# Kernel tuning notes

Hardware: AMD Instinct MI355X
Metric: run time of the kernel (lower is better)

The kernel has to match this reference:

```python
import jax, jax.numpy as jnp
import numpy as np

N_NODES = 7823
N_DRUG = 708
N_TARGET = 1512
N_DISEASE = N_NODES - N_DRUG - N_TARGET  # 5603
FEAT = 1024
HID = 512
OUT = 256
LN_EPS = 1e-5


def _adapter_params(key, in_dim, out_dim):
    k1, k2 = jax.random.split(key)
    s1 = (2.0 / (in_dim + out_dim)) ** 0.5
    return dict(
        W=jax.random.normal(k1, (out_dim, in_dim), jnp.float32) * s1,
        b=jnp.zeros((out_dim,), jnp.float32),
        g=jnp.ones((out_dim,), jnp.float32),
        beta=jnp.zeros((out_dim,), jnp.float32),
        Wr=jax.random.normal(k2, (out_dim, in_dim), jnp.float32) * s1,
        br=jnp.zeros((out_dim,), jnp.float32),
    )


def setup_inputs() -> dict:
    key = jax.random.key(0)
    ks = jax.random.split(key, 12)
    inp = {
        'drug_feats': jax.random.normal(ks[0], (N_DRUG, FEAT), jnp.float32),
        'target_feats': jax.random.normal(ks[1], (N_TARGET, FEAT), jnp.float32),
        'disease_feats': jax.random.normal(ks[2], (N_DISEASE, FEAT), jnp.float32),
        'drug_adjs': jax.random.uniform(ks[3], (2, N_NODES, N_NODES), jnp.float32),
        'target_adjs': jax.random.uniform(ks[4], (2, N_NODES, N_NODES), jnp.float32),
    }
    # adapters
    for name, k in [('dA', ks[5]), ('tA', ks[6]), ('sA', ks[7])]:
        p = _adapter_params(k, FEAT, HID)
        for pn, pv in p.items():
            inp[name + '_' + pn] = pv
    # GCN weights: gc1 [HID,OUT], gc2 [OUT,OUT], uniform(-1/sqrt(out),1/sqrt(out))
    stdv = 1.0 / (OUT ** 0.5)
    inp['dG_W1'] = jax.random.uniform(ks[8], (HID, OUT), jnp.float32, -stdv, stdv)
    inp['dG_W2'] = jax.random.uniform(ks[9], (OUT, OUT), jnp.float32, -stdv, stdv)
    inp['tG_W1'] = jax.random.uniform(ks[10], (HID, OUT), jnp.float32, -stdv, stdv)
    inp['tG_W2'] = jax.random.uniform(ks[11], (OUT, OUT), jnp.float32, -stdv, stdv)
    inp['dG_a'] = jnp.full((1,), 0.25, jnp.float32)  # PReLU init
    inp['tG_a'] = jnp.full((1,), 0.25, jnp.float32)
    return inp


def _layernorm(x, g, b):
    m = x.mean(-1, keepdims=True)
    v = x.var(-1, keepdims=True)
    return (x - m) / jnp.sqrt(v + LN_EPS) * g + b


def _adapter(x, W, b, g, beta, Wr, br):
    out = jax.nn.relu(_layernorm(x @ W.T + b, g, beta))
    return out + x @ Wr.T + br


def _prelu(x, a):
    return jnp.where(x >= 0, x, a * x)


def _gcn(x, adj, W1, W2, a):
    h = _prelu(adj @ (x @ W1), a)
    Z = adj @ (h @ W2)
    # nn.LayerNorm(Z.size()) normalizes over the WHOLE tensor, no affine
    return (Z - Z.mean()) / jnp.sqrt(Z.var() + LN_EPS)


def reference(drug_feats, target_feats, disease_feats, drug_adjs, target_adjs,
              dA_W, dA_b, dA_g, dA_beta, dA_Wr, dA_br,
              tA_W, tA_b, tA_g, tA_beta, tA_Wr, tA_br,
              sA_W, sA_b, sA_g, sA_beta, sA_Wr, sA_br,
              dG_W1, dG_W2, dG_a, tG_W1, tG_W2, tG_a):
    h_drug = jax.nn.elu(_adapter(drug_feats, dA_W, dA_b, dA_g, dA_beta, dA_Wr, dA_br))
    h_target = jax.nn.elu(_adapter(target_feats, tA_W, tA_b, tA_g, tA_beta, tA_Wr, tA_br))
    h_disease = jax.nn.elu(_adapter(disease_feats, sA_W, sA_b, sA_g, sA_beta, sA_Wr, sA_br))
    x_all = jnp.concatenate([h_drug, h_target, h_disease], axis=0)  # [7823, HID]
    adj_d = drug_adjs.mean(0)
    adj_t = target_adjs.mean(0)
    z_drug = _gcn(x_all, adj_d, dG_W1, dG_W2, dG_a)[:N_DRUG]
    z_target = _gcn(x_all, adj_t, tG_W1, tG_W2, tG_a)[N_DRUG:N_DRUG + N_TARGET]
    z_drug = z_drug / (jnp.linalg.norm(z_drug, axis=1, keepdims=True) + 1e-8)
    z_target = z_target / (jnp.linalg.norm(z_target, axis=1, keepdims=True) + 1e-8)
    return (z_drug, z_target)
```

## Files before the change

kernel.cpp:

```cpp
#include <hip/hip_runtime.h>
#include <hip/hip_bf16.h>
#include <stdint.h>

typedef __attribute__((ext_vector_type(8))) short short8;
typedef __attribute__((ext_vector_type(4))) float f32x4;

#define N_DRUG 708
#define N_TGT  1512
#define N_NODES 7823
#define N_D_T  2220
#define KPAD   8192
#define MROWP  7936
#define NTOT   2002688
#define NSPLIT 4
#define PLANE  61199329LL
#define ADJSTR ((long long)MROWP*KPAD)
#define BTSTR  ((long long)256*KPAD)
#define PSTR   ((long long)NSPLIT*NTOT)

__device__ __forceinline__ unsigned short f2bf(float f) {
  union { float f; unsigned int i; } v; v.f = f;
  unsigned int r = v.i + 0x7FFF + ((v.i >> 16) & 1);
  return (unsigned short)(r >> 16);
}

__device__ __forceinline__ int4 pack8(const float v[8]) {
  union { int4 i4; unsigned short u[8]; } r;
  #pragma unroll
  for (int j = 0; j < 8; j++) r.u[j] = f2bf(v[j]);
  return r.i4;
}


__global__ __launch_bounds__(256) void cast_wc(
    const float* __restrict__ w0, const float* __restrict__ wr0,
    const float* __restrict__ w1, const float* __restrict__ wr1,
    const float* __restrict__ w2, const float* __restrict__ wr2,
    unsigned short* __restrict__ Wc)
{
  long long i4 = ((long long)blockIdx.x*256 + threadIdx.x)*4;
  int g  = (int)(i4 >> 20);
  int rr = (int)((i4 >> 10) & 1023);
  int c  = (int)(i4 & 1023);
  const float* src = (g==0) ? (rr<512?w0:wr0) : (g==1) ? (rr<512?w1:wr1) : (rr<512?w2:wr2);
  float4 f = *(const float4*)(src + (long long)(rr & 511)*1024 + c);
  ushort4 v; v.x=f2bf(f.x); v.y=f2bf(f.y); v.z=f2bf(f.z); v.w=f2bf(f.w);
  *(ushort4*)&Wc[i4] = v;
}

__global__ __launch_bounds__(256) void transpose_cast(
    const float* __restrict__ src, unsigned short* __restrict__ dst, int R, int C)
{
  int i = blockIdx.x*256 + threadIdx.x;
  if (i >= R*C) return;
  int r = i / C, c = i - r*C;
  dst[c*R + r] = f2bf(src[i]);
}

__global__ __launch_bounds__(256) void mean_cast_row(
    const float* __restrict__ A0, const float* __restrict__ A1,
    unsigned short* __restrict__ D)
{
  int row = blockIdx.x;
  const float* p0 = (blockIdx.y ? A1 : A0) + (long long)row*N_NODES;
  const float* p1 = p0 + PLANE;
  unsigned short* d = D + (long long)blockIdx.y*ADJSTR + (long long)row*KPAD;

  for (int c = threadIdx.x*8; c < 7816; c += 2048) {
    float4 a0 = *(const float4*)(p0+c);
    float4 a1 = *(const float4*)(p0+c+4);
    float4 b0 = *(const float4*)(p1+c);
    float4 b1 = *(const float4*)(p1+c+4);
    float v[8] = {0.5f*(a0.x+b0.x), 0.5f*(a0.y+b0.y), 0.5f*(a0.z+b0.z), 0.5f*(a0.w+b0.w),
                  0.5f*(a1.x+b1.x), 0.5f*(a1.y+b1.y), 0.5f*(a1.z+b1.z), 0.5f*(a1.w+b1.w)};
    *(int4*)(d + c) = pack8(v);
  }
  int t = threadIdx.x;
  if (t < 7) {
    int c = 7816 + t;
    d[c] = f2bf(0.5f*(p0[c] + p1[c]));
  }
}

__global__ __launch_bounds__(512, 2) void spmmK(
    const unsigned short* __restrict__ Abase,
    const unsigned short* __restrict__ Bbase,
    float* __restrict__ parts)
{
  __shared__ __align__(16) unsigned short Bs[2][128*256];

  int bid = (blockIdx.x & 7)*62 + (blockIdx.x >> 3);
  int grp = bid / 62;
  int q   = bid % 62;
  int b  = grp >> 2;
  int ks = grp & 3;
  int mt = q >> 1, nt = q & 1;

  const unsigned short* A  = Abase + b*ADJSTR;
  const unsigned short* BT = Bbase + b*BTSTR;
  int m0 = mt*256, n0 = nt*128;
  int kt0 = ks*32;

  int tid = threadIdx.x, lane = tid & 63, w = tid >> 6;
  int grow = m0 + w*32 + (lane&15);
  long long rA0 = (long long)grow*KPAD + (lane>>4)*8;

  f32x4 acc[2][8] = {};

  int srow[8], sslot[8];
  #pragma unroll
  for (int i=0;i<8;i++){ int c = i*512 + tid; srow[i] = c>>5; sslot[i] = c&31; }

  int4 breg[8];
  auto loadB = [&](int sub){
    long long kb = (long long)kt0*64 + sub*256;
    #pragma unroll
    for (int i=0;i<8;i++)
      breg[i] = *(const int4*)(BT + (long long)(n0+srow[i])*KPAD + kb + sslot[i]*8);
  };
  auto storeB = [&](unsigned short* buf){
    #pragma unroll
    for (int i=0;i<8;i++)
      *(int4*)(buf + srow[i]*256 + (sslot[i]^(srow[i]&7))*8) = breg[i];
  };
  auto loadA = [&](int g, int4* a){
    const unsigned short* p = A + rA0 + (long long)g*64;
    a[0] = *(const int4*)(p);
    a[1] = *(const int4*)(p + 16*KPAD);
    a[2] = *(const int4*)(p + 32);
    a[3] = *(const int4*)(p + 16*KPAD + 32);
  };
  auto compute = [&](int lt, const int4* a, const unsigned short* buf){
    #pragma unroll
    for (int kk=0; kk<2; ++kk) {
      short8 bv[8];
      #pragma unroll
      for (int nf=0; nf<8; ++nf) {
        int row = nf*16 + (lane&15);
        int sl  = (lt*8 + kk*4 + (lane>>4)) ^ (lane&7);
        bv[nf] = *(const short8*)&buf[row*256 + sl*8];
      }
      #pragma unroll
      for (int mf=0; mf<2; ++mf) {
        short8 av = *(const short8*)&a[kk*2+mf];
        #pragma unroll
        for (int nf=0; nf<8; ++nf)
          acc[mf][nf] = __builtin_amdgcn_mfma_f32_16x16x32_bf16(av, bv[nf], acc[mf][nf], 0, 0, 0);
      }
    }
  };

  int gmax = kt0 + 31;
  int4 a0[4], a1[4], a2[4], a3[4];

  loadB(0);
  loadA(kt0+0, a0);
  loadA(kt0+1, a1);
  loadA(kt0+2, a2);
  loadA(kt0+3, a3);
  storeB(&Bs[0][0]);
  loadB(1);
  asm volatile("s_waitcnt lgkmcnt(0)" ::: "memory");
  __builtin_amdgcn_s_barrier();
  __builtin_amdgcn_sched_barrier(0);

  int cur = 0;
  for (int sub = 0; sub < 8; ++sub) {
    const unsigned short* Bc = &Bs[cur][0];
    int g = kt0 + sub*4;
    compute(0, a0, Bc); loadA(min(g+4, gmax), a0);
    compute(1, a1, Bc); loadA(min(g+5, gmax), a1);
    compute(2, a2, Bc); loadA(min(g+6, gmax), a2);
    compute(3, a3, Bc); loadA(min(g+7, gmax), a3);
    if (sub < 7) {
      __builtin_amdgcn_s_barrier();
      __builtin_amdgcn_sched_barrier(0);
      storeB(&Bs[cur^1][0]);
      loadB(min(sub+2, 7));
      asm volatile("s_waitcnt lgkmcnt(0)" ::: "memory");
      __builtin_amdgcn_s_barrier();
      __builtin_amdgcn_sched_barrier(0);
      cur ^= 1;
    }
  }

  float* P = parts + b*PSTR + (long long)ks*NTOT;
  #pragma unroll
  for (int mf=0; mf<2; ++mf) {
    int mb = m0 + w*32 + mf*16 + ((lane>>4)<<2);
    #pragma unroll
    for (int i=0;i<4;i++){
      int m = mb + i;
      if (m < N_NODES) {
        #pragma unroll
        for (int nf=0; nf<8; ++nf) {
          int n = n0 + nf*16 + (lane&15);
          P[(long long)m*256 + n] = acc[mf][nf][i];
        }
      }
    }
  }
}

#define BN 256
#define BK 64

__global__ __launch_bounds__(512, 4) void gemmS(
    const unsigned short* __restrict__ Abase, long long a_bstr, int lda,
    const unsigned short* __restrict__ Bbase, long long b_bstr, int ldb,
    int m_cnt, int tiles_m, int ktiles,
    unsigned short* __restrict__ CTb, long long ct_bstr, int ldct)
{
  __shared__ __align__(16) unsigned short As[64*BK];
  __shared__ __align__(16) unsigned short Bs[BN*BK];

  int bid = blockIdx.x;
  int b   = bid / tiles_m;
  int tm  = bid % tiles_m;

  const unsigned short* A  = Abase + b*a_bstr;
  const unsigned short* BT = Bbase + b*b_bstr;

  int m0 = tm*64;
  int tid = threadIdx.x;
  int lane = tid & 63, w = tid >> 6;
  int wm = (w >> 2)*32, wn = (w & 3)*64;

  f32x4 acc[2][4] = {};

  int arow, aslot, brow[4], bslot[4];
  { int c = tid; arow = c>>3; aslot = c&7; }
  #pragma unroll
  for (int i=0;i<4;i++){ int c = i*512 + tid; brow[i] = c>>3; bslot[i] = c&7; }

  int4 ra, rb[4];
  auto loadAB = [&](int kt){
    int gr = m0 + arow; if (gr > m_cnt-1) gr = m_cnt-1;
    ra = *(const int4*)(A + (long long)gr*lda + kt*BK + aslot*8);
    #pragma unroll
    for (int i=0;i<4;i++)
      rb[i] = *(const int4*)(BT + (long long)brow[i]*ldb + kt*BK + bslot[i]*8);
  };
  auto storeAB = [&](){
    *(int4*)(As + arow*BK + (aslot^(arow&7))*8) = ra;
    #pragma unroll
    for (int i=0;i<4;i++)
      *(int4*)(Bs + brow[i]*BK + (bslot[i]^(brow[i]&7))*8) = rb[i];
  };

  loadAB(0);
  for (int kt = 0; kt < ktiles; ++kt) {
    __syncthreads();
    storeAB();
    __syncthreads();
    if (kt+1 < ktiles) loadAB(kt+1);
    #pragma unroll
    for (int kk=0; kk<2; ++kk) {
      short8 av[2], bv[4];
      #pragma unroll
      for (int x=0;x<2;x++){
        int row = wm + x*16 + (lane&15);
        int slot = kk*4 + (lane>>4);
        av[x] = *(const short8*)&As[row*BK + (slot^(row&7))*8];
      }
      #pragma unroll
      for (int x=0;x<4;x++){
        int row = wn + x*16 + (lane&15);
        int slot = kk*4 + (lane>>4);
        bv[x] = *(const short8*)&Bs[row*BK + (slot^(row&7))*8];
      }
      #pragma unroll
      for (int mf=0; mf<2; ++mf)
        #pragma unroll
        for (int nf=0; nf<4; ++nf)
          acc[mf][nf] = __builtin_amdgcn_mfma_f32_16x16x32_bf16(av[mf], bv[nf], acc[mf][nf], 0, 0, 0);
    }
  }

  unsigned short* CT = CTb + b*ct_bstr;
  #pragma unroll
  for (int nf=0; nf<4; ++nf) {
    int n = wn + nf*16 + (lane&15);
    #pragma unroll
    for (int mf=0; mf<2; ++mf) {
      int mb = m0 + wm + mf*16 + ((lane>>4)<<2);
      ushort4 v;
      v.x = (mb+0 < m_cnt) ? f2bf(acc[mf][nf][0]) : (unsigned short)0;
      v.y = (mb+1 < m_cnt) ? f2bf(acc[mf][nf][1]) : (unsigned short)0;
      v.z = (mb+2 < m_cnt) ? f2bf(acc[mf][nf][2]) : (unsigned short)0;
      v.w = (mb+3 < m_cnt) ? f2bf(acc[mf][nf][3]) : (unsigned short)0;
      *(ushort4*)&CT[(long long)n*ldct + mb] = v;
    }
  }
}

__global__ __launch_bounds__(512, 4) void adapt_gemm(
    const float* __restrict__ f0, const float* __restrict__ f1, const float* __restrict__ f2,
    const unsigned short* __restrict__ Wc, float* __restrict__ C1)
{
  __shared__ __align__(16) unsigned short As[64*BK];
  __shared__ __align__(16) unsigned short Bs[BN*BK];

  int bid = blockIdx.x;
  int tn = bid & 3, tq = bid >> 2;
  int g, lt, m_cnt, gstart;
  if (tq < 12)      { g=0; lt=tq;    m_cnt=N_DRUG;           gstart=0; }
  else if (tq < 36) { g=1; lt=tq-12; m_cnt=N_TGT;            gstart=N_DRUG; }
  else              { g=2; lt=tq-36; m_cnt=N_NODES-N_D_T;    gstart=N_D_T; }
  const float* A = (g==0) ? f0 : (g==1) ? f1 : f2;
  const unsigned short* BT = Wc + (long long)g*1024*1024;

  int m0 = lt*64, n0 = tn*BN;
  int tid = threadIdx.x;
  int lane = tid & 63, w = tid >> 6;
  int wm = (w >> 2)*32, wn = (w & 3)*64;

  f32x4 acc[2][4] = {};

  int arow, aslot, brow[4], bslot[4];
  { int c = tid; arow = c>>3; aslot = c&7; }
  #pragma unroll
  for (int i=0;i<4;i++){ int c = i*512 + tid; brow[i] = c>>3; bslot[i] = c&7; }

  int4 ra, rb[4];
  auto loadAB = [&](int kt){
    int gr = m0 + arow; if (gr > m_cnt-1) gr = m_cnt-1;
    const float* p = A + (long long)gr*1024 + kt*BK + aslot*8;
    float4 q0 = *(const float4*)p;
    float4 q1 = *(const float4*)(p+4);
    float v[8] = {q0.x,q0.y,q0.z,q0.w,q1.x,q1.y,q1.z,q1.w};
    ra = pack8(v);
    #pragma unroll
    for (int i=0;i<4;i++)
      rb[i] = *(const int4*)(BT + (long long)(n0 + brow[i])*1024 + kt*BK + bslot[i]*8);
  };
  auto storeAB = [&](){
    *(int4*)(As + arow*BK + (aslot^(arow&7))*8) = ra;
    #pragma unroll
    for (int i=0;i<4;i++)
      *(int4*)(Bs + brow[i]*BK + (bslot[i]^(brow[i]&7))*8) = rb[i];
  };

  loadAB(0);
  for (int kt = 0; kt < 16; ++kt) {
    __syncthreads();
    storeAB();
    __syncthreads();
    if (kt+1 < 16) loadAB(kt+1);
    #pragma unroll
    for (int kk=0; kk<2; ++kk) {
      short8 av[2], bv[4];
      #pragma unroll
      for (int x=0;x<2;x++){
        int row = wm + x*16 + (lane&15);
        int slot = kk*4 + (lane>>4);
        av[x] = *(const short8*)&As[row*BK + (slot^(row&7))*8];
      }
      #pragma unroll
      for (int x=0;x<4;x++){
        int row = wn + x*16 + (lane&15);
        int slot = kk*4 + (lane>>4);
        bv[x] = *(const short8*)&Bs[row*BK + (slot^(row&7))*8];
      }
      #pragma unroll
      for (int mf=0; mf<2; ++mf)
        #pragma unroll
        for (int nf=0; nf<4; ++nf)
          acc[mf][nf] = __builtin_amdgcn_mfma_f32_16x16x32_bf16(av[mf], bv[nf], acc[mf][nf], 0, 0, 0);
    }
  }

  #pragma unroll
  for (int mf=0; mf<2; ++mf) {
    int mb = m0 + wm + mf*16 + ((lane>>4)<<2);
    #pragma unroll
    for (int i=0;i<4;i++){
      int m = mb + i;
      if (m < m_cnt) {
        #pragma unroll
        for (int nf=0; nf<4; ++nf) {
          int n = n0 + wn + nf*16 + (lane&15);
          C1[(long long)(gstart+m)*1024 + n] = acc[mf][nf][i];
        }
      }
    }
  }
}


__global__ __launch_bounds__(256) void adapter_fuse(
    const float* __restrict__ C1,
    const float* __restrict__ b0, const float* __restrict__ g0, const float* __restrict__ be0, const float* __restrict__ br0,
    const float* __restrict__ b1, const float* __restrict__ g1, const float* __restrict__ be1, const float* __restrict__ br1,
    const float* __restrict__ b2, const float* __restrict__ g2, const float* __restrict__ be2, const float* __restrict__ br2,
    unsigned short* __restrict__ xall)
{
  int r = blockIdx.x;
  const float *b, *g, *be, *br;
  if (r < N_DRUG)     { b=b0; g=g0; be=be0; br=br0; }
  else if (r < N_D_T) { b=b1; g=g1; be=be1; br=br1; }
  else                { b=b2; g=g2; be=be2; br=br2; }
  int t = threadIdx.x;
  const float* row = C1 + (long long)r*1024;
  float ya = row[t]       + b[t];
  float yb = row[t + 256] + b[t + 256];
  float s = ya + yb, q = ya*ya + yb*yb;
  #pragma unroll
  for (int o=32;o;o>>=1){ s += __shfl_down(s,o); q += __shfl_down(q,o); }
  __shared__ float ss[4], qq[4];
  if ((t & 63) == 0) { ss[t>>6]=s; qq[t>>6]=q; }
  __syncthreads();
  float S = ss[0]+ss[1]+ss[2]+ss[3];
  float Q = qq[0]+qq[1]+qq[2]+qq[3];
  float mean = S * (1.f/512.f);
  float var  = Q * (1.f/512.f) - mean*mean;
  float inv  = rsqrtf(var + 1e-5f);
  float za = fmaxf((ya-mean)*inv*g[t]     + be[t],     0.f);
  float zb = fmaxf((yb-mean)*inv*g[t+256] + be[t+256], 0.f);
  float ha = za + row[512 + t] + br[t];
  float hb = zb + row[768 + t] + br[t + 256];
  ha = (ha > 0.f) ? ha : (expf(ha) - 1.f);
  hb = (hb > 0.f) ? hb : (expf(hb) - 1.f);
  xall[(long long)r*512 + t]       = f2bf(ha);
  xall[(long long)r*512 + t + 256] = f2bf(hb);
}

__global__ __launch_bounds__(256) void reduce_prelu2(
    const float* __restrict__ parts, const float* __restrict__ a0, const float* __restrict__ a1,
    unsigned short* __restrict__ h)
{
  int b = blockIdx.y;
  long long i = (long long)blockIdx.x*256 + threadIdx.x;
  const float* P = parts + b*PSTR;
  float s = 0.f;
  #pragma unroll
  for (int p=0;p<NSPLIT;p++) s += P[(long long)p*NTOT + i];
  float a = (b ? a1 : a0)[0];
  h[b*(long long)NTOT + i] = f2bf(s >= 0.f ? s : a*s);
}

__global__ __launch_bounds__(256) void reduce_stats2(
    const float* __restrict__ parts, float* __restrict__ Z, float* __restrict__ sp)
{
  int b = blockIdx.y;
  long long i = (long long)blockIdx.x*256 + threadIdx.x;
  const float* P = parts + b*PSTR;
  float s = 0.f;
  #pragma unroll
  for (int p=0;p<NSPLIT;p++) s += P[(long long)p*NTOT + i];
  Z[b*(long long)NTOT + i] = s;
  float a = s, q = s*s;
  #pragma unroll
  for (int o=32;o;o>>=1){ a += __shfl_down(a,o); q += __shfl_down(q,o); }
  __shared__ float ss[4], qq[4];
  int t = threadIdx.x;
  if ((t&63)==0){ ss[t>>6]=a; qq[t>>6]=q; }
  __syncthreads();
  if (t==0) {
    sp[(long long)b*2*N_NODES + 2*blockIdx.x]   = ss[0]+ss[1]+ss[2]+ss[3];
    sp[(long long)b*2*N_NODES + 2*blockIdx.x+1] = qq[0]+qq[1]+qq[2]+qq[3];
  }
}

__global__ __launch_bounds__(256) void stats_final2(
    const float* __restrict__ sp, float* __restrict__ stats)
{
  int b = blockIdx.x;
  const float* S = sp + (long long)b*2*N_NODES;
  int t = threadIdx.x;
  float s = 0.f, q = 0.f;
  for (int i=t; i<N_NODES; i+=256){ s += S[2*i]; q += S[2*i+1]; }
  #pragma unroll
  for (int o=32;o;o>>=1){ s += __shfl_down(s,o); q += __shfl_down(q,o); }
  __shared__ float ss[4], qq[4];
  if ((t&63)==0){ ss[t>>6]=s; qq[t>>6]=q; }
  __syncthreads();
  if (t==0){ stats[b*16]=ss[0]+ss[1]+ss[2]+ss[3]; stats[b*16+1]=qq[0]+qq[1]+qq[2]+qq[3]; }
}

__global__ __launch_bounds__(256) void finalize(
    const float* __restrict__ Z, const float* __restrict__ stats,
    float* __restrict__ out, int row_lo, long long out_off)
{
  int r = row_lo + blockIdx.x;
  int t = threadIdx.x;
  float mean = stats[0] * (1.f/(float)NTOT);
  float var  = stats[1] * (1.f/(float)NTOT) - mean*mean;
  float inv  = rsqrtf(var + 1e-5f);
  float z = (Z[(long long)r*256 + t] - mean) * inv;
  float q = z*z;
  #pragma unroll
  for (int o=32;o;o>>=1) q += __shfl_down(q,o);
  __shared__ float qq[4];
  if ((t&63)==0) qq[t>>6]=q;
  __syncthreads();
  float norm = sqrtf(qq[0]+qq[1]+qq[2]+qq[3]);
  out[out_off + (long long)blockIdx.x*256 + t] = z / (norm + 1e-8f);
}


extern "C" void kernel_launch(void* const* d_in, const int* in_sizes, int n_in,
                              void* d_out, int out_size, void* d_ws, size_t ws_size,
                              hipStream_t stream)
{
  const float* drug_feats    = (const float*)d_in[0];
  const float* target_feats  = (const float*)d_in[1];
  const float* disease_feats = (const float*)d_in[2];
  const float* drug_adjs     = (const float*)d_in[3];
  const float* target_adjs   = (const float*)d_in[4];
  const float* dA_W  = (const float*)d_in[5];
  const float* dA_b  = (const float*)d_in[6];
  const float* dA_g  = (const float*)d_in[7];
  const float* dA_be = (const float*)d_in[8];
  const float* dA_Wr = (const float*)d_in[9];
  const float* dA_br = (const float*)d_in[10];
  const float* tA_W  = (const float*)d_in[11];
  const float* tA_b  = (const float*)d_in[12];
  const float* tA_g  = (const float*)d_in[13];
  const float* tA_be = (const float*)d_in[14];
  const float* tA_Wr = (const float*)d_in[15];
  const float* tA_br = (const float*)d_in[16];
  const float* sA_W  = (const float*)d_in[17];
  const float* sA_b  = (const float*)d_in[18];
  const float* sA_g  = (const float*)d_in[19];
  const float* sA_be = (const float*)d_in[20];
  const float* sA_Wr = (const float*)d_in[21];
  const float* sA_br = (const float*)d_in[22];
  const float* dG_W1 = (const float*)d_in[23];
  const float* dG_W2 = (const float*)d_in[24];
  const float* tG_W1 = (const float*)d_in[25];
  const float* tG_W2 = (const float*)d_in[26];
  const float* dG_a  = (const float*)d_in[27];
  const float* tG_a  = (const float*)d_in[28];

  char* ws = (char*)d_ws;
  size_t off = 0;
  auto alloc = [&](size_t bytes)->void* {
    void* p = ws + off;
    off += (bytes + 255) & ~(size_t)255;
    return p;
  };

  unsigned short* Wc   = (unsigned short*)alloc((size_t)3*1024*1024*2);
  unsigned short* W1T  = (unsigned short*)alloc((size_t)2*256*512*2);
  unsigned short* W2T  = (unsigned short*)alloc((size_t)2*256*256*2);
  unsigned short* xall = (unsigned short*)alloc((size_t)N_NODES*512*2);
  unsigned short* adjb = (unsigned short*)alloc((size_t)2*ADJSTR*2);
  unsigned short* xw1T = (unsigned short*)alloc((size_t)2*BTSTR*2);
  unsigned short* hbuf = (unsigned short*)alloc((size_t)2*NTOT*2);
  unsigned short* hw2T = (unsigned short*)alloc((size_t)2*BTSTR*2);
  float* parts = (float*)alloc((size_t)2*PSTR*4);
  float* Zf    = (float*)alloc((size_t)2*NTOT*4);
  float* spart = (float*)alloc((size_t)2*N_NODES*2*4);
  float* stats = (float*)alloc((size_t)32*4);
  float* C1    = parts;
  float* outp  = (float*)d_out;

  cast_wc<<<3072, 256, 0, stream>>>(dA_W, dA_Wr, tA_W, tA_Wr, sA_W, sA_Wr, Wc);
  transpose_cast<<<512, 256, 0, stream>>>(dG_W1, W1T,            512, 256);
  transpose_cast<<<512, 256, 0, stream>>>(tG_W1, W1T + 256*512,  512, 256);
  transpose_cast<<<256, 256, 0, stream>>>(dG_W2, W2T,            256, 256);
  transpose_cast<<<256, 256, 0, stream>>>(tG_W2, W2T + 256*256,  256, 256);

  adapt_gemm<<<496, 512, 0, stream>>>(drug_feats, target_feats, disease_feats, Wc, C1);
  adapter_fuse<<<N_NODES, 256, 0, stream>>>(C1,
      dA_b, dA_g, dA_be, dA_br,
      tA_b, tA_g, tA_be, tA_br,
      sA_b, sA_g, sA_be, sA_br, xall);

  gemmS<<<2*128, 512, 0, stream>>>(
      xall, 0, 512, W1T, 256*512, 512,
      N_NODES, 128, 8, xw1T, BTSTR, KPAD);

  mean_cast_row<<<dim3(N_NODES, 2), 256, 0, stream>>>(drug_adjs, target_adjs, adjb);

  spmmK<<<496, 512, 0, stream>>>(adjb, xw1T, parts);

  reduce_prelu2<<<dim3(N_NODES,2), 256, 0, stream>>>(parts, dG_a, tG_a, hbuf);

  gemmS<<<2*128, 512, 0, stream>>>(
      hbuf, (long long)NTOT, 256, W2T, 256*256, 256,
      N_NODES, 128, 4, hw2T, BTSTR, KPAD);

  spmmK<<<496, 512, 0, stream>>>(adjb, hw2T, parts);

  reduce_stats2<<<dim3(N_NODES,2), 256, 0, stream>>>(parts, Zf, spart);
  stats_final2<<<2, 256, 0, stream>>>(spart, stats);

  finalize<<<N_DRUG, 256, 0, stream>>>(Zf, stats, outp, 0, 0LL);
  finalize<<<N_TGT, 256, 0, stream>>>(Zf + NTOT, stats + 16, outp, N_DRUG, (long long)N_DRUG*256);
}
```

Before: 841.4 us.

## Drop split-K in adjacency GEMMs and fuse PReLU/stats epilogues

```diff
diff --git a/kernel.cpp b/kernel.cpp
--- a/kernel.cpp
+++ b/kernel.cpp
@@ -12,11 +12,9 @@
 #define KPAD   8192
 #define MROWP  7936
 #define NTOT   2002688
-#define NSPLIT 4
 #define PLANE  61199329LL
 #define ADJSTR ((long long)MROWP*KPAD)
 #define BTSTR  ((long long)256*KPAD)
-#define PSTR   ((long long)NSPLIT*NTOT)
 
 __device__ __forceinline__ unsigned short f2bf(float f) {
   union { float f; unsigned int i; } v; v.f = f;
@@ -82,46 +80,47 @@
   }
 }
 
-__global__ __launch_bounds__(512, 2) void spmmK(
+template<int TYPE>
+__global__ __launch_bounds__(512, 2) void spmmT(
     const unsigned short* __restrict__ Abase,
     const unsigned short* __restrict__ Bbase,
-    float* __restrict__ parts)
-{
-  __shared__ __align__(16) unsigned short Bs[2][128*256];
-
-  int bid = (blockIdx.x & 7)*62 + (blockIdx.x >> 3);
-  int grp = bid / 62;
-  int q   = bid % 62;
-  int b  = grp >> 2;
-  int ks = grp & 3;
-  int mt = q >> 1, nt = q & 1;
+    const float* __restrict__ al0, const float* __restrict__ al1,
+    unsigned short* __restrict__ Hb,
+    float* __restrict__ Zf, float* __restrict__ spart)
+{
+  __shared__ __align__(16) unsigned short Bs[2][256*128];
+  __shared__ float rs[8], rq[8];
+
+  int bid = (blockIdx.x & 7)*31 + (blockIdx.x >> 3);
+  int b  = bid / 124;
+  int mt = bid % 124;
 
   const unsigned short* A  = Abase + b*ADJSTR;
   const unsigned short* BT = Bbase + b*BTSTR;
-  int m0 = mt*256, n0 = nt*128;
-  int kt0 = ks*32;
+  int m0 = mt*64;
 
   int tid = threadIdx.x, lane = tid & 63, w = tid >> 6;
-  int grow = m0 + w*32 + (lane&15);
+  int wm = (w>>2)*32, wn = (w&3)*64;
+  int grow = m0 + wm + (lane&15);
   long long rA0 = (long long)grow*KPAD + (lane>>4)*8;
 
-  f32x4 acc[2][8] = {};
+  f32x4 acc[2][4] = {};
 
   int srow[8], sslot[8];
   #pragma unroll
-  for (int i=0;i<8;i++){ int c = i*512 + tid; srow[i] = c>>5; sslot[i] = c&31; }
+  for (int i=0;i<8;i++){ int c = i*512 + tid; srow[i] = c>>4; sslot[i] = c&15; }
 
   int4 breg[8];
   auto loadB = [&](int sub){
-    long long kb = (long long)kt0*64 + sub*256;
+    long long kb = (long long)sub*128;
     #pragma unroll
     for (int i=0;i<8;i++)
-      breg[i] = *(const int4*)(BT + (long long)(n0+srow[i])*KPAD + kb + sslot[i]*8);
+      breg[i] = *(const int4*)(BT + (long long)srow[i]*KPAD + kb + sslot[i]*8);
   };
   auto storeB = [&](unsigned short* buf){
     #pragma unroll
     for (int i=0;i<8;i++)
-      *(int4*)(buf + srow[i]*256 + (sslot[i]^(srow[i]&7))*8) = breg[i];
+      *(int4*)(buf + srow[i]*128 + (sslot[i]^(srow[i]&7))*8) = breg[i];
   };
   auto loadA = [&](int g, int4* a){
     const unsigned short* p = A + rA0 + (long long)g*64;
@@ -133,31 +132,30 @@
   auto compute = [&](int lt, const int4* a, const unsigned short* buf){
     #pragma unroll
     for (int kk=0; kk<2; ++kk) {
-      short8 bv[8];
-      #pragma unroll
-      for (int nf=0; nf<8; ++nf) {
-        int row = nf*16 + (lane&15);
+      short8 bv[4];
+      #pragma unroll
+      for (int nf=0; nf<4; ++nf) {
+        int row = wn + nf*16 + (lane&15);
         int sl  = (lt*8 + kk*4 + (lane>>4)) ^ (lane&7);
-        bv[nf] = *(const short8*)&buf[row*256 + sl*8];
+        bv[nf] = *(const short8*)&buf[row*128 + sl*8];
       }
       #pragma unroll
       for (int mf=0; mf<2; ++mf) {
         short8 av = *(const short8*)&a[kk*2+mf];
         #pragma unroll
-        for (int nf=0; nf<8; ++nf)
+        for (int nf=0; nf<4; ++nf)
           acc[mf][nf] = __builtin_amdgcn_mfma_f32_16x16x32_bf16(av, bv[nf], acc[mf][nf], 0, 0, 0);
       }
     }
   };
 
-  int gmax = kt0 + 31;
   int4 a0[4], a1[4], a2[4], a3[4];
 
   loadB(0);
-  loadA(kt0+0, a0);
-  loadA(kt0+1, a1);
-  loadA(kt0+2, a2);
-  loadA(kt0+3, a3);
+  loadA(0, a0);
+  loadA(1, a1);
+  loadA(2, a2);
+  loadA(3, a3);
   storeB(&Bs[0][0]);
   loadB(1);
   asm volatile("s_waitcnt lgkmcnt(0)" ::: "memory");
@@ -165,39 +163,84 @@
   __builtin_amdgcn_sched_barrier(0);
 
   int cur = 0;
-  for (int sub = 0; sub < 8; ++sub) {
-    const unsigned short* Bc = &Bs[cur][0];
-    int g = kt0 + sub*4;
-    compute(0, a0, Bc); loadA(min(g+4, gmax), a0);
-    compute(1, a1, Bc); loadA(min(g+5, gmax), a1);
-    compute(2, a2, Bc); loadA(min(g+6, gmax), a2);
-    compute(3, a3, Bc); loadA(min(g+7, gmax), a3);
-    if (sub < 7) {
-      __builtin_amdgcn_s_barrier();
-      __builtin_amdgcn_sched_barrier(0);
+  #pragma unroll 1
+  for (int sp = 0; sp < 32; ++sp) {
+    int g = sp*4;
+    {
+      const unsigned short* Bc = &Bs[cur][0];
+      compute(0, a0, Bc); loadA(min(g+4, 127), a0);
+      compute(1, a1, Bc); loadA(min(g+5, 127), a1);
       storeB(&Bs[cur^1][0]);
-      loadB(min(sub+2, 7));
+      loadB(min(2*sp+2, 63));
       asm volatile("s_waitcnt lgkmcnt(0)" ::: "memory");
       __builtin_amdgcn_s_barrier();
       __builtin_amdgcn_sched_barrier(0);
       cur ^= 1;
     }
-  }
-
-  float* P = parts + b*PSTR + (long long)ks*NTOT;
-  #pragma unroll
-  for (int mf=0; mf<2; ++mf) {
-    int mb = m0 + w*32 + mf*16 + ((lane>>4)<<2);
-    #pragma unroll
-    for (int i=0;i<4;i++){
-      int m = mb + i;
-      if (m < N_NODES) {
-        #pragma unroll
-        for (int nf=0; nf<8; ++nf) {
-          int n = n0 + nf*16 + (lane&15);
-          P[(long long)m*256 + n] = acc[mf][nf][i];
+    {
+      const unsigned short* Bc = &Bs[cur][0];
+      compute(0, a2, Bc); loadA(min(g+6, 127), a2);
+      compute(1, a3, Bc); loadA(min(g+7, 127), a3);
+      if (sp < 31) {
+        storeB(&Bs[cur^1][0]);
+        loadB(min(2*sp+3, 63));
+        asm volatile("s_waitcnt lgkmcnt(0)" ::: "memory");
+        __builtin_amdgcn_s_barrier();
+        __builtin_amdgcn_sched_barrier(0);
+        cur ^= 1;
+      }
+    }
+  }
+
+  if (TYPE == 0) {
+    float alpha = (b ? al1 : al0)[0];
+    unsigned short* H = Hb + (long long)b*NTOT;
+    #pragma unroll
+    for (int mf=0; mf<2; ++mf) {
+      int mb = m0 + wm + mf*16 + ((lane>>4)<<2);
+      #pragma unroll
+      for (int i=0;i<4;i++){
+        int m = mb + i;
+        if (m < N_NODES) {
+          #pragma unroll
+          for (int nf=0; nf<4; ++nf) {
+            int n = wn + nf*16 + (lane&15);
+            float s = acc[mf][nf][i];
+            H[(long long)m*256 + n] = f2bf(s >= 0.f ? s : alpha*s);
+          }
         }
       }
+    }
+  } else {
+    float* Z = Zf + (long long)b*NTOT;
+    float ls = 0.f, lq = 0.f;
+    #pragma unroll
+    for (int mf=0; mf<2; ++mf) {
+      int mb = m0 + wm + mf*16 + ((lane>>4)<<2);
+      #pragma unroll
+      for (int i=0;i<4;i++){
+        int m = mb + i;
+        if (m < N_NODES) {
+          #pragma unroll
+          for (int nf=0; nf<4; ++nf) {
+            int n = wn + nf*16 + (lane&15);
+            float s = acc[mf][nf][i];
+            Z[(long long)m*256 + n] = s;
+            ls += s; lq += s*s;
+          }
+        }
+      }
+    }
+    #pragma unroll
+    for (int o=32;o;o>>=1){ ls += __shfl_down(ls,o); lq += __shfl_down(lq,o); }
+    if (lane == 0) { rs[w] = ls; rq[w] = lq; }
+    __syncthreads();
+    if (tid == 0) {
+      float S=0.f, Q=0.f;
+      #pragma unroll
+      for (int i=0;i<8;i++){ S += rs[i]; Q += rq[i]; }
+      spart[(b*124 + mt)*2]     = S;
+      spart[(b*124 + mt)*2 + 1] = Q;
     }
   }
 }
@@ -425,51 +468,13 @@
   xall[(long long)r*512 + t + 256] = f2bf(hb);
 }
 
-__global__ __launch_bounds__(256) void reduce_prelu2(
-    const float* __restrict__ parts, const float* __restrict__ a0, const float* __restrict__ a1,
-    unsigned short* __restrict__ h)
-{
-  int b = blockIdx.y;
-  long long i = (long long)blockIdx.x*256 + threadIdx.x;
-  const float* P = parts + b*PSTR;
-  float s = 0.f;
-  #pragma unroll
-  for (int p=0;p<NSPLIT;p++) s += P[(long long)p*NTOT + i];
-  float a = (b ? a1 : a0)[0];
-  h[b*(long long)NTOT + i] = f2bf(s >= 0.f ? s : a*s);
-}
-
-__global__ __launch_bounds__(256) void reduce_stats2(
-    const float* __restrict__ parts, float* __restrict__ Z, float* __restrict__ sp)
-{
-  int b = blockIdx.y;
-  long long i = (long long)blockIdx.x*256 + threadIdx.x;
-  const float* P = parts + b*PSTR;
-  float s = 0.f;
-  #pragma unroll
-  for (int p=0;p<NSPLIT;p++) s += P[(long long)p*NTOT + i];
-  Z[b*(long long)NTOT + i] = s;
-  float a = s, q = s*s;
-  #pragma unroll
-  for (int o=32;o;o>>=1){ a += __shfl_down(a,o); q += __shfl_down(q,o); }
-  __shared__ float ss[4], qq[4];
-  int t = threadIdx.x;
-  if ((t&63)==0){ ss[t>>6]=a; qq[t>>6]=q; }
-  __syncthreads();
-  if (t==0) {
-    sp[(long long)b*2*N_NODES + 2*blockIdx.x]   = ss[0]+ss[1]+ss[2]+ss[3];
-    sp[(long long)b*2*N_NODES + 2*blockIdx.x+1] = qq[0]+qq[1]+qq[2]+qq[3];
-  }
-}
-
 __global__ __launch_bounds__(256) void stats_final2(
     const float* __restrict__ sp, float* __restrict__ stats)
 {
   int b = blockIdx.x;
-  const float* S = sp + (long long)b*2*N_NODES;
   int t = threadIdx.x;
   float s = 0.f, q = 0.f;
-  for (int i=t; i<N_NODES; i+=256){ s += S[2*i]; q += S[2*i+1]; }
+  for (int i=t; i<124; i+=256){ s += sp[(b*124+i)*2]; q += sp[(b*124+i)*2+1]; }
   #pragma unroll
   for (int o=32;o;o>>=1){ s += __shfl_down(s,o); q += __shfl_down(q,o); }
   __shared__ float ss[4], qq[4];
@@ -549,11 +554,10 @@
   unsigned short* xw1T = (unsigned short*)alloc((size_t)2*BTSTR*2);
   unsigned short* hbuf = (unsigned short*)alloc((size_t)2*NTOT*2);
   unsigned short* hw2T = (unsigned short*)alloc((size_t)2*BTSTR*2);
-  float* parts = (float*)alloc((size_t)2*PSTR*4);
+  float* C1    = (float*)alloc((size_t)N_NODES*1024*4);
   float* Zf    = (float*)alloc((size_t)2*NTOT*4);
-  float* spart = (float*)alloc((size_t)2*N_NODES*2*4);
+  float* spart = (float*)alloc((size_t)2*124*2*4);
   float* stats = (float*)alloc((size_t)32*4);
-  float* C1    = parts;
   float* outp  = (float*)d_out;
 
   cast_wc<<<3072, 256, 0, stream>>>(dA_W, dA_Wr, tA_W, tA_Wr, sA_W, sA_Wr, Wc);
@@ -574,17 +578,14 @@
 
   mean_cast_row<<<dim3(N_NODES, 2), 256, 0, stream>>>(drug_adjs, target_adjs, adjb);
 
-  spmmK<<<496, 512, 0, stream>>>(adjb, xw1T, parts);
-
-  reduce_prelu2<<<dim3(N_NODES,2), 256, 0, stream>>>(parts, dG_a, tG_a, hbuf);
+  spmmT<0><<<248, 512, 0, stream>>>(adjb, xw1T, dG_a, tG_a, hbuf, nullptr, nullptr);
 
   gemmS<<<2*128, 512, 0, stream>>>(
       hbuf, (long long)NTOT, 256, W2T, 256*256, 256,
       N_NODES, 128, 4, hw2T, BTSTR, KPAD);
 
-  spmmK<<<496, 512, 0, stream>>>(adjb, hw2T, parts);
-
-  reduce_stats2<<<dim3(N_NODES,2), 256, 0, stream>>>(parts, Zf, spart);
+  spmmT<1><<<248, 512, 0, stream>>>(adjb, hw2T, nullptr, nullptr, nullptr, Zf, spart);
+
   stats_final2<<<2, 256, 0, stream>>>(spart, stats);
 
   finalize<<<N_DRUG, 256, 0, stream>>>(Zf, stats, outp, 0, 0LL);
```

Measured after the change: 1.350 ms. 60.5% more time.

## Retile spmmK to 128x256 output blocks with deeper B prefetch

Applied to the files above, without the earlier changes.

```diff
diff --git a/kernel.cpp b/kernel.cpp
--- a/kernel.cpp
+++ b/kernel.cpp
@@ -87,41 +87,41 @@
     const unsigned short* __restrict__ Bbase,
     float* __restrict__ parts)
 {
-  __shared__ __align__(16) unsigned short Bs[2][128*256];
+  __shared__ __align__(16) unsigned short Bs[2][256*128];
 
   int bid = (blockIdx.x & 7)*62 + (blockIdx.x >> 3);
   int grp = bid / 62;
-  int q   = bid % 62;
+  int mt  = bid % 62;
   int b  = grp >> 2;
   int ks = grp & 3;
-  int mt = q >> 1, nt = q & 1;
 
   const unsigned short* A  = Abase + b*ADJSTR;
   const unsigned short* BT = Bbase + b*BTSTR;
-  int m0 = mt*256, n0 = nt*128;
+  int m0 = mt*128;
   int kt0 = ks*32;
 
   int tid = threadIdx.x, lane = tid & 63, w = tid >> 6;
-  int grow = m0 + w*32 + (lane&15);
+  int wm = (w>>1)*32, wn = (w&1)*128;
+  int grow = m0 + wm + (lane&15);
   long long rA0 = (long long)grow*KPAD + (lane>>4)*8;
 
   f32x4 acc[2][8] = {};
 
   int srow[8], sslot[8];
   #pragma unroll
-  for (int i=0;i<8;i++){ int c = i*512 + tid; srow[i] = c>>5; sslot[i] = c&31; }
-
-  int4 breg[8];
-  auto loadB = [&](int sub){
-    long long kb = (long long)kt0*64 + sub*256;
+  for (int i=0;i<8;i++){ int c = i*512 + tid; srow[i] = c>>4; sslot[i] = c&15; }
+
+  int4 bregA[8], bregB[8];
+  auto loadB = [&](int sub, int4* br){
+    long long kb = (long long)kt0*64 + sub*128;
     #pragma unroll
     for (int i=0;i<8;i++)
-      breg[i] = *(const int4*)(BT + (long long)(n0+srow[i])*KPAD + kb + sslot[i]*8);
-  };
-  auto storeB = [&](unsigned short* buf){
+      br[i] = *(const int4*)(BT + (long long)srow[i]*KPAD + kb + sslot[i]*8);
+  };
+  auto storeB = [&](unsigned short* buf, const int4* br){
     #pragma unroll
     for (int i=0;i<8;i++)
-      *(int4*)(buf + srow[i]*256 + (sslot[i]^(srow[i]&7))*8) = breg[i];
+      *(int4*)(buf + srow[i]*128 + (sslot[i]^(srow[i]&7))*8) = br[i];
   };
   auto loadA = [&](int g, int4* a){
     const unsigned short* p = A + rA0 + (long long)g*64;
@@ -136,9 +136,9 @@
       short8 bv[8];
       #pragma unroll
       for (int nf=0; nf<8; ++nf) {
-        int row = nf*16 + (lane&15);
+        int row = wn + nf*16 + (lane&15);
         int sl  = (lt*8 + kk*4 + (lane>>4)) ^ (lane&7);
-        bv[nf] = *(const short8*)&buf[row*256 + sl*8];
+        bv[nf] = *(const short8*)&buf[row*128 + sl*8];
       }
       #pragma unroll
       for (int mf=0; mf<2; ++mf) {
@@ -153,48 +153,63 @@
   int gmax = kt0 + 31;
   int4 a0[4], a1[4], a2[4], a3[4];
 
-  loadB(0);
+  loadB(0, bregA);
   loadA(kt0+0, a0);
   loadA(kt0+1, a1);
   loadA(kt0+2, a2);
   loadA(kt0+3, a3);
-  storeB(&Bs[0][0]);
-  loadB(1);
+  storeB(&Bs[0][0], bregA);
+  loadB(1, bregA);
+  loadB(2, bregB);
   asm volatile("s_waitcnt lgkmcnt(0)" ::: "memory");
   __builtin_amdgcn_s_barrier();
   __builtin_amdgcn_sched_barrier(0);
 
   int cur = 0;
-  for (int sub = 0; sub < 8; ++sub) {
-    const unsigned short* Bc = &Bs[cur][0];
-    int g = kt0 + sub*4;
-    compute(0, a0, Bc); loadA(min(g+4, gmax), a0);
-    compute(1, a1, Bc); loadA(min(g+5, gmax), a1);
-    compute(2, a2, Bc); loadA(min(g+6, gmax), a2);
-    compute(3, a3, Bc); loadA(min(g+7, gmax), a3);
-    if (sub < 7) {
+  #pragma unroll 1
+  for (int sp = 0; sp < 8; ++sp) {
+    int g = kt0 + sp*4;
+    {
+      const unsigned short* Bc = &Bs[cur][0];
+      compute(0, a0, Bc); loadA(min(g+4, gmax), a0);
+      compute(1, a1, Bc); loadA(min(g+5, gmax), a1);
       __builtin_amdgcn_s_barrier();
       __builtin_amdgcn_sched_barrier(0);
-      storeB(&Bs[cur^1][0]);
-      loadB(min(sub+2, 7));
+      storeB(&Bs[cur^1][0], bregA);
+      loadB(min(2*sp+3, 15), bregA);
       asm volatile("s_waitcnt lgkmcnt(0)" ::: "memory");
       __builtin_amdgcn_s_barrier();
       __builtin_amdgcn_sched_barrier(0);
       cur ^= 1;
     }
+    {
+      const unsigned short* Bc = &Bs[cur][0];
+      compute(0, a2, Bc); loadA(min(g+6, gmax), a2);
+      compute(1, a3, Bc); loadA(min(g+7, gmax), a3);
+      if (sp < 7) {
+        __builtin_amdgcn_s_barrier();
+        __builtin_amdgcn_sched_barrier(0);
+        storeB(&Bs[cur^1][0], bregB);
+        loadB(min(2*sp+4, 15), bregB);
+        asm volatile("s_waitcnt lgkmcnt(0)" ::: "memory");
+        __builtin_amdgcn_s_barrier();
+        __builtin_amdgcn_sched_barrier(0);
+        cur ^= 1;
+      }
+    }
   }
 
   float* P = parts + b*PSTR + (long long)ks*NTOT;
   #pragma unroll
   for (int mf=0; mf<2; ++mf) {
-    int mb = m0 + w*32 + mf*16 + ((lane>>4)<<2);
+    int mb = m0 + wm + mf*16 + ((lane>>4)<<2);
     #pragma unroll
     for (int i=0;i<4;i++){
       int m = mb + i;
       if (m < N_NODES) {
         #pragma unroll
         for (int nf=0; nf<8; ++nf) {
-          int n = n0 + nf*16 + (lane&15);
+          int n = wn + nf*16 + (lane&15);
           P[(long long)m*256 + n] = acc[mf][nf][i];
         }
       }
```

Result: slower. 1.025 ms (+21.8%).
